# Performance work log

Hardware: AMD Instinct MI355X
Metric: run time of the kernel (lower is better)

## Reference

```python
import jax, jax.numpy as jnp
import numpy as np

N = 100_000      # nodes
E = 1_600_000    # edges (avg degree 16)
C_IN = 128
HID = 128        # 2 * out_channels
OUT = 64
EDIM = 1
NEG_SLOPE = 0.2  # PyG GATConv default negative_slope


def _gat(x, src, dst, n, W, a_s, a_d, b, edge_attr=None, We=None, a_e=None):
    """PyG GATConv with heads=1, concat=True, add_self_loops=True (fill_value='mean').
    x: [n, Cin]; src/dst: [E] (messages flow src -> dst); returns [n, Cout].
    """
    xl = x @ W                 # [n, Cout] transformed node features
    a_src = xl @ a_s           # [n] per-node source attention logit
    a_dst = xl @ a_d           # [n] per-node destination attention logit
    loop = jnp.arange(n)
    if edge_attr is not None:
        # self-loop edge_attr = mean of incoming edge_attr per node (fill_value='mean')
        ones = jnp.ones((src.shape[0],), xl.dtype)
        cnt = jax.ops.segment_sum(ones, dst, num_segments=n)              # [n]
        s = jax.ops.segment_sum(edge_attr, dst, num_segments=n)           # [n, EDIM]
        loop_attr = jnp.where(cnt[:, None] > 0, s / jnp.maximum(cnt, 1.0)[:, None], 0.0)
        ea = jnp.concatenate([edge_attr, loop_attr], axis=0)              # [E+n, EDIM]
    src2 = jnp.concatenate([src, loop])
    dst2 = jnp.concatenate([dst, loop])
    alpha = a_src[src2] + a_dst[dst2]                                      # [E+n]
    if edge_attr is not None:
        alpha = alpha + (ea @ We) @ a_e                                    # edge-attribute attention term
    alpha = jax.nn.leaky_relu(alpha, NEG_SLOPE)
    # softmax over incoming edges of each destination node (stable)
    m = jax.ops.segment_max(alpha, dst2, num_segments=n)
    ex = jnp.exp(alpha - m[dst2])
    den = jax.ops.segment_sum(ex, dst2, num_segments=n)
    coef = ex / den[dst2]                                                  # [E+n]
    out = jax.ops.segment_sum(coef[:, None] * xl[src2], dst2, num_segments=n)
    return out + b


def setup_inputs() -> dict:
    key = jax.random.key(0)
    ks = jax.random.split(key, 32)
    s = 0.1
    inp = {
        "x": jax.random.normal(ks[0], (N, C_IN), jnp.float32),
        "edge_index": jax.random.randint(ks[1], (2, E), 0, N, jnp.int64),
        "edge_weights": jax.random.uniform(ks[2], (E, EDIM), jnp.float32),
    }
    def lin(k, i, o):
        return jax.random.normal(k, (i, o), jnp.float32) * s
    def vec(k, c):
        return jax.random.normal(k, (c,), jnp.float32) * s
    # layer 0: 128 -> 128 (with edge attention)
    inp["W0"], inp["as0"], inp["ad0"] = lin(ks[3], C_IN, HID), vec(ks[4], HID), vec(ks[5], HID)
    inp["ae0"], inp["We0"], inp["b0"] = vec(ks[6], HID), lin(ks[7], EDIM, HID), jnp.zeros((HID,), jnp.float32)
    # layer 1: 128 -> 128 (with edge attention)
    inp["W1"], inp["as1"], inp["ad1"] = lin(ks[8], HID, HID), vec(ks[9], HID), vec(ks[10], HID)
    inp["ae1"], inp["We1"], inp["b1"] = vec(ks[11], HID), lin(ks[12], EDIM, HID), jnp.zeros((HID,), jnp.float32)
    # conv_mu: 128 -> 64 (with edge attention)
    inp["Wm"], inp["asm"], inp["adm"] = lin(ks[13], HID, OUT), vec(ks[14], OUT), vec(ks[15], OUT)
    inp["aem"], inp["Wem"], inp["bm"] = vec(ks[16], OUT), lin(ks[17], EDIM, OUT), jnp.zeros((OUT,), jnp.float32)
    # conv_logstd: 128 -> 64 (called WITHOUT edge_attr -> no edge term)
    inp["Wl"], inp["asl"], inp["adl"] = lin(ks[18], HID, OUT), vec(ks[19], OUT), vec(ks[20], OUT)
    inp["bl"] = jnp.zeros((OUT,), jnp.float32)
    return inp


def reference(x, edge_index, edge_weights,
              W0, as0, ad0, ae0, We0, b0,
              W1, as1, ad1, ae1, We1, b1,
              Wm, asm, adm, aem, Wem, bm,
              Wl, asl, adl, bl):
    src, dst = edge_index[0], edge_index[1]
    h = jax.nn.relu(_gat(x, src, dst, N, W0, as0, ad0, b0, edge_weights, We0, ae0))
    h = jax.nn.relu(_gat(h, src, dst, N, W1, as1, ad1, b1, edge_weights, We1, ae1))
    mu = _gat(h, src, dst, N, Wm, asm, adm, bm, edge_weights, Wem, aem)
    logstd = _gat(h, src, dst, N, Wl, asl, adl, bl)  # no edge_attr, per original forward
    return mu, logstd
```

## Files before the change

### kernel.cpp

```cpp
#include <hip/hip_runtime.h>

#define NN 100000
#define EE 1600000
#define NBK 782
#define NBKP 784
#define NBLK 391
#define NBLKP 392

typedef __attribute__((ext_vector_type(8))) __bf16 bf16x8;
typedef __attribute__((ext_vector_type(4))) float f32x4;
typedef unsigned short u16;

__device__ __forceinline__ float bf2f(u16 v) {
  union { unsigned u; float f; } x; x.u = ((unsigned)v) << 16; return x.f;
}
__device__ __forceinline__ u16 f2bf(float f) {
  union { unsigned u; float f; } x; x.f = f;
  x.u += 0x7fffu + ((x.u >> 16) & 1u);
  return (u16)(x.u >> 16);
}
__device__ __forceinline__ float lo_f(unsigned u) {
  union { unsigned u; float f; } x; x.u = u << 16; return x.f;
}
__device__ __forceinline__ float hi_f(unsigned u) {
  union { unsigned u; float f; } x; x.u = u & 0xffff0000u; return x.f;
}
__device__ __forceinline__ unsigned pack2(float a, float b) {
  return (unsigned)f2bf(a) | ((unsigned)f2bf(b) << 16);
}
__device__ __forceinline__ float lrelu(float x) { return x > 0.f ? x : 0.2f * x; }
__device__ __forceinline__ int clampi(int v, int hi) {
  return ((unsigned)v < (unsigned)hi) ? v : 0;
}
__device__ __forceinline__ float ldf(const void* p, size_t i, int fl) {
  return fl ? ((const float*)p)[i] : bf2f(((const u16*)p)[i]);
}

__device__ __forceinline__ int wave_fdetect(const u16* __restrict__ xb) {
  int lane = threadIdx.x & 63;
  int bad = 0;
#pragma unroll
  for (int j = 0; j < 4; ++j) {
    float a = fabsf(bf2f(xb[lane * 4 + j]));
    bad |= (!(a == a) || a > 1e6f) ? 1 : 0;
  }
  return (__ballot(bad) != 0ull) ? 1 : 0;
}
__device__ __forceinline__ int wave_mdetect(const int* __restrict__ ei) {
  int lane = threadIdx.x & 63;
  int v = (lane < 32) ? ei[2 * lane + 1] : 0;
  return (__ballot(v != 0) == 0ull) ? 1 : 0;
}

__global__ void k_fillf(float* __restrict__ o, int n, float v) {
  int i = blockIdx.x * 256 + threadIdx.x;
  if (i < n) o[i] = v;
}

struct CvtDesc { const void* src; u16* dst; int n; };
struct SetupArgs {
  CvtDesc cvt[12];
  const void* W[4]; u16* WT[4]; int WM[4];
  const void* dw[3]; const void* da[3]; int dm[3];
  float* cvals;
  const u16* xb;
};
__global__ __launch_bounds__(256) void k_setup(SetupArgs a) {
  int b = blockIdx.x, t = threadIdx.x;
  if (b < 12) {
    int fl = wave_fdetect(a.xb);
    const void* src = a.cvt[b].src; u16* dst = a.cvt[b].dst; int n = a.cvt[b].n;
    for (int i = t; i < n; i += 256)
      dst[i] = fl ? f2bf(((const float*)src)[i]) : ((const u16*)src)[i];
    return;
  }
  b -= 12;
  if (b < 192) {
    int fl = wave_fdetect(a.xb);
    int wsel, lb;
    if (b < 64)       { wsel = 0; lb = b; }
    else if (b < 128) { wsel = 1; lb = b - 64; }
    else if (b < 160) { wsel = 2; lb = b - 128; }
    else              { wsel = 3; lb = b - 160; }
    int M = a.WM[wsel];
    int i = lb * 256 + t;
    if (i < 128 * M) {
      int k = i / M, m = i % M;
      a.WT[wsel][m * 128 + k] = f2bf(ldf(a.W[wsel], i, fl));
    }
    return;
  }
  b -= 192;
  if (b < 3) {
    if (t < 64) {
      int fl = wave_fdetect(a.xb);
      float s = 0.f; int m = a.dm[b];
      for (int j = t; j < m; j += 64) s += ldf(a.dw[b], j, fl) * ldf(a.da[b], j, fl);
      for (int off = 32; off; off >>= 1) s += __shfl_xor(s, off);
      if (t == 0) a.cvals[b] = s;
    }
    return;
  }
}

__global__ __launch_bounds__(256) void k_ehist(const int* __restrict__ ei,
                                               int* __restrict__ histM) {
  __shared__ int h[NBKP];
  int blk = blockIdx.x, t = threadIdx.x;
  int m_ = wave_mdetect(ei);
  for (int j = t; j < NBKP; j += 256) h[j] = 0;
  __syncthreads();
#pragma unroll
  for (int j = 0; j < 16; ++j) {
    int e = blk * 4096 + j * 256 + t;
    if (e < EE) {
      int d = m_ ? ei[2 * (size_t)(EE + e)] : ei[EE + e];
      d = clampi(d, NN);
      atomicAdd(&h[d >> 7], 1);
    }
  }
  __syncthreads();
  for (int j = t; j < NBKP; j += 256) histM[j * NBLKP + blk] = h[j];
}

__global__ __launch_bounds__(512) void k_scanA(int* __restrict__ histM,
                                               int* __restrict__ binTot) {
  int b = blockIdx.x, t = threadIdx.x;
  int v = (t < NBLK) ? histM[b * NBLKP + t] : 0;
  int lane = t & 63, w = t >> 6;
  int sc = v;
  for (int off = 1; off < 64; off <<= 1) {
    int o = __shfl_up(sc, off); if (lane >= off) sc += o;
  }
  __shared__ int wt[8];
  if (lane == 63) wt[w] = sc;
  __syncthreads();
  int add = 0;
  for (int k = 0; k < w; ++k) add += wt[k];
  int excl = sc - v + add;
  if (t < NBLK) histM[b * NBLKP + t] = excl;
  if (t == 511) binTot[b] = excl;
}

__global__ __launch_bounds__(256) void k_scanB(const int* __restrict__ binTot,
                                               int* __restrict__ bucketBase,
                                               int* __restrict__ row_off) {
  int t = threadIdx.x;
  int v[4]; int s = 0;
#pragma unroll
  for (int j = 0; j < 4; ++j) {
    int idx = t * 4 + j;
    v[j] = (idx < NBK) ? binTot[idx] : 0;
    s += v[j];
  }
  int lane = t & 63, w = t >> 6;
  int sc = s;
  for (int off = 1; off < 64; off <<= 1) {
    int o = __shfl_up(sc, off); if (lane >= off) sc += o;
  }
  __shared__ int wt[4];
  if (lane == 63) wt[w] = sc;
  __syncthreads();
  int add = 0;
  for (int k = 0; k < w; ++k) add += wt[k];
  int ex = add + sc - s;
#pragma unroll
  for (int j = 0; j < 4; ++j) {
    int idx = t * 4 + j;
    if (idx <= NBK) bucketBase[idx] = ex;
    ex += v[j];
  }
  if (t == 0) row_off[NN] = EE;
}

__global__ __launch_bounds__(256) void k_escatter(
    const int* __restrict__ ei, const void* __restrict__ ew,
    const u16* __restrict__ xb, const int* __restrict__ histM,
    const int* __restrict__ bucketBase, int2* __restrict__ stage) {
  __shared__ int lbase[NBKP];
  __shared__ int cur[NBKP];
  int blk = blockIdx.x, t = threadIdx.x;
  int m_ = wave_mdetect(ei);
  int fl = wave_fdetect(xb);
  for (int j = t; j < NBKP; j += 256) {
    int bb = (j < NBK) ? (bucketBase[j] + histM[j * NBLKP + blk]) : 0;
    lbase[j] = bb; cur[j] = 0;
  }
  __syncthreads();
#pragma unroll
  for (int j = 0; j < 16; ++j) {
    int e = blk * 4096 + j * 256 + t;
    if (e < EE) {
      int s = m_ ? ei[2 * (size_t)e] : ei[e];
      int d = m_ ? ei[2 * (size_t)(EE + e)] : ei[EE + e];
      s = clampi(s, NN);
      d = clampi(d, NN);
      int bin = d >> 7, low = d & 127;
      int r = atomicAdd(&cur[bin], 1);
      int pos = lbase[bin] + r;
      if (pos >= 0 && pos < EE)
        stage[pos] = make_int2(s, (low << 16) | (int)f2bf(ldf(ew, e, fl)));
    }
  }
}

__global__ __launch_bounds__(256) void k_bucket(
    const int2* __restrict__ stage, const int* __restrict__ bucketBase,
    int2* __restrict__ edges, int* __restrict__ row_off, float* __restrict__ la) {
  __shared__ int hist[128];
  __shared__ float wsum[128];
  __shared__ int pref[128];
  __shared__ int cur[128];
  int b = blockIdx.x, t = threadIdx.x;
  int base = bucketBase[b], n = bucketBase[b + 1] - base;
  if (t < 128) { hist[t] = 0; wsum[t] = 0.f; cur[t] = 0; }
  __syncthreads();
  for (int i = t; i < n; i += 256) {
    int2 it = stage[base + i];
    int bin = (it.y >> 16) & 127;
    atomicAdd(&hist[bin], 1);
    atomicAdd(&wsum[bin], bf2f((u16)(it.y & 0xffff)));
  }
  __syncthreads();
  if (t == 0) {
    int run = 0;
    for (int j = 0; j < 128; ++j) { pref[j] = run; run += hist[j]; }
  }
  __syncthreads();
  if (t < 128) {
    int d = b * 128 + t;
    if (d < NN) {
      row_off[d] = base + pref[t];
      la[d] = hist[t] ? wsum[t] / (float)hist[t] : 0.f;
    }
  }
  for (int i = t; i < n; i += 256) {
    int2 it = stage[base + i];
    int bin = (it.y >> 16) & 127;
    int r = atomicAdd(&cur[bin], 1);
    edges[base + pref[bin] + r] = it;
  }
}

template<bool DUAL>
__device__ __forceinline__ void gemm_body(
    int bid, int fl, const void* __restrict__ Araw,
    const u16* __restrict__ WT,
    const u16* __restrict__ avs, const u16* __restrict__ avd,
    u16* __restrict__ xl,
    float* __restrict__ asrc, float* __restrict__ adst,
    float2* __restrict__ asAB, float* __restrict__ adstB, int n) {
  const int K = 128;
  int lane = threadIdx.x & 63;
  int wave = threadIdx.x >> 6;
  int quad = lane >> 4;
  int l16 = lane & 15;
  int r0 = (bid * 4 + wave) * 16;
  if (r0 >= n) return;
  int arow = r0 + l16; if (arow >= n) arow = n - 1;
  bf16x8 afr[4];
  if (fl) {
    const float* af = (const float*)Araw + (size_t)arow * K + quad * 8;
#pragma unroll
    for (int kb = 0; kb < 4; ++kb) {
      float4 f0 = *(const float4*)(af + kb * 32);
      float4 f1 = *(const float4*)(af + kb * 32 + 4);
      union { bf16x8 v; u16 s[8]; } t;
      t.s[0] = f2bf(f0.x); t.s[1] = f2bf(f0.y); t.s[2] = f2bf(f0.z); t.s[3] = f2bf(f0.w);
      t.s[4] = f2bf(f1.x); t.s[5] = f2bf(f1.y); t.s[6] = f2bf(f1.z); t.s[7] = f2bf(f1.w);
      afr[kb] = t.v;
    }
  } else {
    const u16* ab = (const u16*)Araw + (size_t)arow * K + quad * 8;
#pragma unroll
    for (int kb = 0; kb < 4; ++kb) afr[kb] = *(const bf16x8*)(ab + kb * 32);
  }
  f32x4 acc[8];
#pragma unroll
  for (int nb = 0; nb < 8; ++nb) acc[nb] = (f32x4){0.f, 0.f, 0.f, 0.f};
#pragma unroll
  for (int nb = 0; nb < 8; ++nb) {
    const u16* bbase = WT + (size_t)(nb * 16 + l16) * K + quad * 8;
#pragma unroll
    for (int kb = 0; kb < 4; ++kb) {
      bf16x8 bfr = *(const bf16x8*)(bbase + kb * 32);
      acc[nb] = __builtin_amdgcn_mfma_f32_16x16x32_bf16(afr[kb], bfr, acc[nb], 0, 0, 0);
    }
  }
  float ps[2][4] = {{0,0,0,0},{0,0,0,0}}, pd[2][4] = {{0,0,0,0},{0,0,0,0}};
#pragma unroll
  for (int nb = 0; nb < 8; ++nb) {
    const int g = (DUAL && nb >= 4) ? 1 : 0;
    int col = nb * 16 + l16;
    float vs = bf2f(avs[col]), vd = bf2f(avd[col]);
#pragma unroll
    for (int r = 0; r < 4; ++r) {
      int row = r0 + quad * 4 + r;
      float v = acc[nb][r];
      if (row < n) xl[(size_t)row * 128 + col] = f2bf(v);
      ps[g][r] += v * vs;
      pd[g][r] += v * vd;
    }
  }
#pragma unroll
  for (int off = 1; off < 16; off <<= 1) {
#pragma unroll
    for (int r = 0; r < 4; ++r) {
      ps[0][r] += __shfl_xor(ps[0][r], off);
      pd[0][r] += __shfl_xor(pd[0][r], off);
      if (DUAL) {
        ps[1][r] += __shfl_xor(ps[1][r], off);
        pd[1][r] += __shfl_xor(pd[1][r], off);
      }
    }
  }
  if (l16 == 0) {
#pragma unroll
    for (int r = 0; r < 4; ++r) {
      int row = r0 + quad * 4 + r;
      if (row < n) {
        if (DUAL) {
          asAB[row] = make_float2(ps[0][r], ps[1][r]);
          adst[row] = pd[0][r]; adstB[row] = pd[1][r];
        } else {
          asrc[row] = ps[0][r]; adst[row] = pd[0][r];
        }
      }
    }
  }
}

__global__ __launch_bounds__(256) void k_gemm0(
    const u16* __restrict__ xb, const void* __restrict__ Araw,
    const u16* __restrict__ WT, const u16* __restrict__ avs, const u16* __restrict__ avd,
    u16* __restrict__ xl, float* __restrict__ asrc, float* __restrict__ adst, int n) {
  int fl = wave_fdetect(xb);
  gemm_body<false>(blockIdx.x, fl, Araw, WT, avs, avd, xl, asrc, adst,
                   nullptr, nullptr, n);
}

template<bool DUAL>
__global__ __launch_bounds__(256) void k_gemm(
    const u16* __restrict__ A, const u16* __restrict__ WT,
    const u16* __restrict__ avs, const u16* __restrict__ avd,
    u16* __restrict__ xl, float* __restrict__ asrc, float* __restrict__ adst,
    float2* __restrict__ asAB, float* __restrict__ adstB, int n) {
  gemm_body<DUAL>(blockIdx.x, 0, A, WT, avs, avd, xl, asrc, adst, asAB, adstB, n);
}

__global__ __launch_bounds__(256) void k_agg(
    const int* __restrict__ row_off, const int2* __restrict__ edges,
    const float* __restrict__ asrc, const float* __restrict__ adst,
    const float* __restrict__ la, const float* __restrict__ cptr,
    const u16* __restrict__ xl, const u16* __restrict__ bias,
    u16* __restrict__ out, int n) {
  __shared__ float lp[16][16];
  __shared__ int lsv[16][16];
  int tid = blockIdx.x * 256 + threadIdx.x;
  int d = tid >> 4;
  if (d >= n) return;
  int l = threadIdx.x & 15;
  int grp = threadIdx.x >> 4;
  float c = cptr[0];
  float ad = adst[d];
  float aL = lrelu(asrc[d] + ad + c * la[d]);
  float lsum = 0.f;
  int4 su = *(const int4*)(xl + (size_t)d * 128 + l * 8);
  float A0 = lo_f(su.x), A1 = hi_f(su.x), A2 = lo_f(su.y), A3 = hi_f(su.y);
  float A4 = lo_f(su.z), A5 = hi_f(su.z), A6 = lo_f(su.w), A7 = hi_f(su.w);
  float B0 = 0.f, B1 = 0.f, B2 = 0.f, B3 = 0.f, B4 = 0.f, B5 = 0.f, B6 = 0.f, B7 = 0.f;
  int beg = row_off[d], end = row_off[d + 1];
  for (int base = beg; base < end; base += 16) {
    int i = base + l;
    bool v = i < end;
    int2 ev = v ? edges[i] : make_int2(0, 0);
    float e = 0.f;
    if (v) e = __expf(lrelu(asrc[ev.x] + ad + c * bf2f((u16)(ev.y & 0xffff))) - aL);
    lsum += e;
    lp[grp][l] = e; lsv[grp][l] = ev.x;
    int cnt = end - base; if (cnt > 16) cnt = 16;
    int j = 0;
    for (; j + 2 <= cnt; j += 2) {
      float p0 = lp[grp][j];     int s0 = lsv[grp][j];
      float p1 = lp[grp][j + 1]; int s1 = lsv[grp][j + 1];
      int4 u0 = *(const int4*)(xl + (size_t)s0 * 128 + l * 8);
      int4 u1 = *(const int4*)(xl + (size_t)s1 * 128 + l * 8);
      A0 = fmaf(p0, lo_f(u0.x), A0); A1 = fmaf(p0, hi_f(u0.x), A1);
      A2 = fmaf(p0, lo_f(u0.y), A2); A3 = fmaf(p0, hi_f(u0.y), A3);
      A4 = fmaf(p0, lo_f(u0.z), A4); A5 = fmaf(p0, hi_f(u0.z), A5);
      A6 = fmaf(p0, lo_f(u0.w), A6); A7 = fmaf(p0, hi_f(u0.w), A7);
      B0 = fmaf(p1, lo_f(u1.x), B0); B1 = fmaf(p1, hi_f(u1.x), B1);
      B2 = fmaf(p1, lo_f(u1.y), B2); B3 = fmaf(p1, hi_f(u1.y), B3);
      B4 = fmaf(p1, lo_f(u1.z), B4); B5 = fmaf(p1, hi_f(u1.z), B5);
      B6 = fmaf(p1, lo_f(u1.w), B6); B7 = fmaf(p1, hi_f(u1.w), B7);
    }
    if (j < cnt) {
      float p0 = lp[grp][j]; int s0 = lsv[grp][j];
      int4 u0 = *(const int4*)(xl + (size_t)s0 * 128 + l * 8);
      A0 = fmaf(p0, lo_f(u0.x), A0); A1 = fmaf(p0, hi_f(u0.x), A1);
      A2 = fmaf(p0, lo_f(u0.y), A2); A3 = fmaf(p0, hi_f(u0.y), A3);
      A4 = fmaf(p0, lo_f(u0.z), A4); A5 = fmaf(p0, hi_f(u0.z), A5);
      A6 = fmaf(p0, lo_f(u0.w), A6); A7 = fmaf(p0, hi_f(u0.w), A7);
    }
  }
  A0 += B0; A1 += B1; A2 += B2; A3 += B3; A4 += B4; A5 += B5; A6 += B6; A7 += B7;
#pragma unroll
  for (int off = 1; off < 16; off <<= 1) lsum += __shfl_xor(lsum, off);
  float inv = 1.f / (lsum + 1.f);
  int4 bv = *(const int4*)(bias + l * 8);
  float o0 = fmaxf(fmaf(A0, inv, lo_f((unsigned)bv.x)), 0.f);
  float o1 = fmaxf(fmaf(A1, inv, hi_f((unsigned)bv.x)), 0.f);
  float o2 = fmaxf(fmaf(A2, inv, lo_f((unsigned)bv.y)), 0.f);
  float o3 = fmaxf(fmaf(A3, inv, hi_f((unsigned)bv.y)), 0.f);
  float o4 = fmaxf(fmaf(A4, inv, lo_f((unsigned)bv.z)), 0.f);
  float o5 = fmaxf(fmaf(A5, inv, hi_f((unsigned)bv.z)), 0.f);
  float o6 = fmaxf(fmaf(A6, inv, lo_f((unsigned)bv.w)), 0.f);
  float o7 = fmaxf(fmaf(A7, inv, hi_f((unsigned)bv.w)), 0.f);
  int4 ov;
  ov.x = (int)pack2(o0, o1); ov.y = (int)pack2(o2, o3);
  ov.z = (int)pack2(o4, o5); ov.w = (int)pack2(o6, o7);
  *(int4*)(out + (size_t)d * 128 + l * 8) = ov;
}

__global__ __launch_bounds__(256) void k_aggh(
    const int* __restrict__ row_off, const int2* __restrict__ edges,
    const float2* __restrict__ asAB, const float* __restrict__ adA,
    const float* __restrict__ adB,
    const float* __restrict__ la, const float* __restrict__ cptr,
    const u16* __restrict__ xl, const u16* __restrict__ bias,
    float* __restrict__ outf, int n) {
  __shared__ float lpA[16][16];
  __shared__ float lpB[16][16];
  __shared__ int lsv[16][16];
  int tid = blockIdx.x * 256 + threadIdx.x;
  int d = tid >> 4;
  if (d >= n) return;
  int l = threadIdx.x & 15;
  int grp = threadIdx.x >> 4;
  bool isMu = l < 8;
  float c = cptr[0];
  float adAd = adA[d], adBd = adB[d];
  float2 abd = asAB[d];
  float aLA = lrelu(abd.x + adAd + c * la[d]);
  float aLB = lrelu(abd.y + adBd);
  float lsA = 0.f, lsB = 0.f;
  int4 su = *(const int4*)(xl + (size_t)d * 128 + l * 8);
  float A0 = lo_f(su.x), A1 = hi_f(su.x), A2 = lo_f(su.y), A3 = hi_f(su.y);
  float A4 = lo_f(su.z), A5 = hi_f(su.z), A6 = lo_f(su.w), A7 = hi_f(su.w);
  float B0 = 0.f, B1 = 0.f, B2 = 0.f, B3 = 0.f, B4 = 0.f, B5 = 0.f, B6 = 0.f, B7 = 0.f;
  int beg = row_off[d], end = row_off[d + 1];
  for (int base = beg; base < end; base += 16) {
    int i = base + l;
    bool v = i < end;
    int2 ev = v ? edges[i] : make_int2(0, 0);
    float eA = 0.f, eB = 0.f;
    if (v) {
      float2 ab = asAB[ev.x];
      eA = __expf(lrelu(ab.x + adAd + c * bf2f((u16)(ev.y & 0xffff))) - aLA);
      eB = __expf(lrelu(ab.y + adBd) - aLB);
    }
    lsA += eA; lsB += eB;
    lpA[grp][l] = eA; lpB[grp][l] = eB; lsv[grp][l] = ev.x;
    const float* lpp = isMu ? lpA[grp] : lpB[grp];
    int cnt = end - base; if (cnt > 16) cnt = 16;
    int j = 0;
    for (; j + 2 <= cnt; j += 2) {
      float p0 = lpp[j];     int s0 = lsv[grp][j];
      float p1 = lpp[j + 1]; int s1 = lsv[grp][j + 1];
      int4 u0 = *(const int4*)(xl + (size_t)s0 * 128 + l * 8);
      int4 u1 = *(const int4*)(xl + (size_t)s1 * 128 + l * 8);
      A0 = fmaf(p0, lo_f(u0.x), A0); A1 = fmaf(p0, hi_f(u0.x), A1);
      A2 = fmaf(p0, lo_f(u0.y), A2); A3 = fmaf(p0, hi_f(u0.y), A3);
      A4 = fmaf(p0, lo_f(u0.z), A4); A5 = fmaf(p0, hi_f(u0.z), A5);
      A6 = fmaf(p0, lo_f(u0.w), A6); A7 = fmaf(p0, hi_f(u0.w), A7);
      B0 = fmaf(p1, lo_f(u1.x), B0); B1 = fmaf(p1, hi_f(u1.x), B1);
      B2 = fmaf(p1, lo_f(u1.y), B2); B3 = fmaf(p1, hi_f(u1.y), B3);
      B4 = fmaf(p1, lo_f(u1.z), B4); B5 = fmaf(p1, hi_f(u1.z), B5);
      B6 = fmaf(p1, lo_f(u1.w), B6); B7 = fmaf(p1, hi_f(u1.w), B7);
    }
    if (j < cnt) {
      float p0 = lpp[j]; int s0 = lsv[grp][j];
      int4 u0 = *(const int4*)(xl + (size_t)s0 * 128 + l * 8);
      A0 = fmaf(p0, lo_f(u0.x), A0); A1 = fmaf(p0, hi_f(u0.x), A1);
      A2 = fmaf(p0, lo_f(u0.y), A2); A3 = fmaf(p0, hi_f(u0.y), A3);
      A4 = fmaf(p0, lo_f(u0.z), A4); A5 = fmaf(p0, hi_f(u0.z), A5);
      A6 = fmaf(p0, lo_f(u0.w), A6); A7 = fmaf(p0, hi_f(u0.w), A7);
    }
  }
  A0 += B0; A1 += B1; A2 += B2; A3 += B3; A4 += B4; A5 += B5; A6 += B6; A7 += B7;
#pragma unroll
  for (int off = 1; off < 16; off <<= 1) {
    lsA += __shfl_xor(lsA, off);
    lsB += __shfl_xor(lsB, off);
  }
  float inv = 1.f / ((isMu ? lsA : lsB) + 1.f);
  int4 bv = *(const int4*)(bias + l * 8);
  float4 oa, ob;
  oa.x = fmaf(A0, inv, lo_f((unsigned)bv.x));
  oa.y = fmaf(A1, inv, hi_f((unsigned)bv.x));
  oa.z = fmaf(A2, inv, lo_f((unsigned)bv.y));
  oa.w = fmaf(A3, inv, hi_f((unsigned)bv.y));
  ob.x = fmaf(A4, inv, lo_f((unsigned)bv.z));
  ob.y = fmaf(A5, inv, hi_f((unsigned)bv.z));
  ob.z = fmaf(A6, inv, lo_f((unsigned)bv.w));
  ob.w = fmaf(A7, inv, hi_f((unsigned)bv.w));
  float* obase = isMu ? (outf + (size_t)d * 64 + l * 8)
                      : (outf + (size_t)NN * 64 + (size_t)d * 64 + (l - 8) * 8);
  *(float4*)obase = oa;
  *(float4*)(obase + 4) = ob;
}

extern "C" void kernel_launch(void* const* d_in, const int* in_sizes, int n_in,
                              void* d_out, int out_size, void* d_ws, size_t ws_size,
                              hipStream_t stream) {
  (void)in_sizes; (void)n_in;
  const int* ei = (const int*)d_in[1];
  const u16* xb = (const u16*)d_in[0];
  float* outf = (float*)d_out;

  u16* regionA = (u16*)d_out;
  u16* regionB = (u16*)d_out + (size_t)NN * 128;
  int* histM = (int*)d_out;

  char* p = (char*)d_ws;
  auto alloc = [&](size_t bytes) -> char* {
    char* r = p; p += (bytes + 255) & ~(size_t)255; return r;
  };
  int*   row_off   = (int*)alloc((NN + 1) * 4);
  int*   binTot    = (int*)alloc(NBKP * 4);
  int*   bucketBase= (int*)alloc((NBKP + 2) * 4);
  float* la        = (float*)alloc(NN * 4);
  float* asrcA     = (float*)alloc(NN * 4);
  float* adstA     = (float*)alloc(NN * 4);
  float* adstB     = (float*)alloc(NN * 4);
  float2* asAB     = (float2*)alloc((size_t)NN * 8);
  int2*  edges     = (int2*)alloc((size_t)EE * 8);
  u16*   WT0       = (u16*)alloc(128 * 128 * 2);
  u16*   WT1       = (u16*)alloc(128 * 128 * 2);
  u16*   WTh       = (u16*)alloc(128 * 128 * 2);
  float* cvals     = (float*)alloc(16);
  u16*   vecc      = (u16*)alloc(9 * 256);
  u16*   xl        = (u16*)alloc((size_t)NN * 128 * 2);

  int2* stage = (int2*)xl;

  size_t NEED = (size_t)(p - (char*)d_ws);
  if (ws_size < NEED) {
    k_fillf<<<(out_size + 255) / 256, 256, 0, stream>>>(outf, out_size, 0.125f);
    return;
  }

  u16* as0c = vecc + 0 * 128; u16* ad0c = vecc + 1 * 128; u16* b0c = vecc + 2 * 128;
  u16* as1c = vecc + 3 * 128; u16* ad1c = vecc + 4 * 128; u16* b1c = vecc + 5 * 128;
  u16* hvs  = vecc + 6 * 128; u16* hvd  = vecc + 7 * 128; u16* bh  = vecc + 8 * 128;

  SetupArgs sa;
  sa.cvt[0]  = {d_in[4],  as0c, 128};
  sa.cvt[1]  = {d_in[5],  ad0c, 128};
  sa.cvt[2]  = {d_in[8],  b0c,  128};
  sa.cvt[3]  = {d_in[10], as1c, 128};
  sa.cvt[4]  = {d_in[11], ad1c, 128};
  sa.cvt[5]  = {d_in[14], b1c,  128};
  sa.cvt[6]  = {d_in[16], hvs,      64};
  sa.cvt[7]  = {d_in[22], hvs + 64, 64};
  sa.cvt[8]  = {d_in[17], hvd,      64};
  sa.cvt[9]  = {d_in[23], hvd + 64, 64};
  sa.cvt[10] = {d_in[20], bh,       64};
  sa.cvt[11] = {d_in[24], bh + 64,  64};
  sa.W[0] = d_in[3];  sa.WT[0] = WT0;            sa.WM[0] = 128;
  sa.W[1] = d_in[9];  sa.WT[1] = WT1;            sa.WM[1] = 128;
  sa.W[2] = d_in[15]; sa.WT[2] = WTh;            sa.WM[2] = 64;
  sa.W[3] = d_in[21]; sa.WT[3] = WTh + 64 * 128; sa.WM[3] = 64;
  sa.dw[0] = d_in[7];  sa.da[0] = d_in[6];  sa.dm[0] = 128;
  sa.dw[1] = d_in[13]; sa.da[1] = d_in[12]; sa.dm[1] = 128;
  sa.dw[2] = d_in[19]; sa.da[2] = d_in[18]; sa.dm[2] = 64;
  sa.cvals = cvals; sa.xb = xb;
  k_setup<<<12 + 192 + 3, 256, 0, stream>>>(sa);

  const int gblocks = (((NN + 15) / 16) + 3) / 4;
  const int eblocks16 = (int)(((size_t)NN * 16 + 255) / 256);

  k_ehist<<<NBLK, 256, 0, stream>>>(ei, histM);
  k_scanA<<<NBK, 512, 0, stream>>>(histM, binTot);
  k_scanB<<<1, 256, 0, stream>>>(binTot, bucketBase, row_off);
  k_escatter<<<NBLK, 256, 0, stream>>>(ei, d_in[2], xb, histM, bucketBase, stage);
  k_bucket<<<NBK, 256, 0, stream>>>(stage, bucketBase, edges, row_off, la);

  k_gemm0<<<gblocks, 256, 0, stream>>>(xb, d_in[0], WT0, as0c, ad0c,
                                       xl, asrcA, adstA, NN);
  k_agg<<<eblocks16, 256, 0, stream>>>(row_off, edges, asrcA, adstA, la,
                                       cvals + 0, xl, b0c, regionB, NN);
  k_gemm<false><<<gblocks, 256, 0, stream>>>(regionB, WT1, as1c, ad1c,
                                             xl, asrcA, adstA, nullptr, nullptr, NN);
  k_agg<<<eblocks16, 256, 0, stream>>>(row_off, edges, asrcA, adstA, la,
                                       cvals + 1, xl, b1c, regionA, NN);
  k_gemm<true><<<gblocks, 256, 0, stream>>>(regionA, WTh, hvs, hvd,
                                            xl, nullptr, adstA, asAB, adstB, NN);
  k_aggh<<<eblocks16, 256, 0, stream>>>(row_off, edges, asAB, adstA, adstB,
                                        la, cvals + 2, xl, bh, outf, NN);
}
```

Baseline: 526.2 us.

## Merge edge histogram into setup and edge scatter with first GEMM launch

Folds the edge-destination histogram blocks into the setup kernel and runs the edge scatter alongside the first-layer GEMM in one launch, which cuts two kernel launches and lets independent work share the GPU. The stage buffer moves from the xl workspace into the output region so the scatter and the GEMM writing xl do not collide. The aggregation kernels also gain a 4-way unrolled gather loop for more memory-level parallelism. Risks include the stage buffer overlapping histM or other output data, and higher register pressure from the wider unroll.

```diff
diff --git a/kernel.cpp b/kernel.cpp
--- a/kernel.cpp
+++ b/kernel.cpp
@@ -6,6 +6,7 @@
 #define NBKP 784
 #define NBLK 391
 #define NBLKP 392
+#define SETB 207
 
 typedef __attribute__((ext_vector_type(8))) __bf16 bf16x8;
 typedef __attribute__((ext_vector_type(4))) float f32x4;
@@ -64,9 +65,30 @@
   const void* dw[3]; const void* da[3]; int dm[3];
   float* cvals;
   const u16* xb;
+  const int* ei;
+  int* histM;
 };
 __global__ __launch_bounds__(256) void k_setup(SetupArgs a) {
+  __shared__ int h[NBKP];
   int b = blockIdx.x, t = threadIdx.x;
+  if (b >= SETB) {
+    int blk = b - SETB;
+    int m_ = wave_mdetect(a.ei);
+    for (int j = t; j < NBKP; j += 256) h[j] = 0;
+    __syncthreads();
+#pragma unroll
+    for (int j = 0; j < 16; ++j) {
+      int e = blk * 4096 + j * 256 + t;
+      if (e < EE) {
+        int d = m_ ? a.ei[2 * (size_t)(EE + e)] : a.ei[EE + e];
+        d = clampi(d, NN);
+        atomicAdd(&h[d >> 7], 1);
+      }
+    }
+    __syncthreads();
+    for (int j = t; j < NBKP; j += 256) a.histM[j * NBLKP + blk] = h[j];
+    return;
+  }
   if (b < 12) {
     int fl = wave_fdetect(a.xb);
     const void* src = a.cvt[b].src; u16* dst = a.cvt[b].dst; int n = a.cvt[b].n;
@@ -103,26 +125,6 @@
   }
 }
 
-__global__ __launch_bounds__(256) void k_ehist(const int* __restrict__ ei,
-                                               int* __restrict__ histM) {
-  __shared__ int h[NBKP];
-  int blk = blockIdx.x, t = threadIdx.x;
-  int m_ = wave_mdetect(ei);
-  for (int j = t; j < NBKP; j += 256) h[j] = 0;
-  __syncthreads();
-#pragma unroll
-  for (int j = 0; j < 16; ++j) {
-    int e = blk * 4096 + j * 256 + t;
-    if (e < EE) {
-      int d = m_ ? ei[2 * (size_t)(EE + e)] : ei[EE + e];
-      d = clampi(d, NN);
-      atomicAdd(&h[d >> 7], 1);
-    }
-  }
-  __syncthreads();
-  for (int j = t; j < NBKP; j += 256) histM[j * NBLKP + blk] = h[j];
-}
-
 __global__ __launch_bounds__(512) void k_scanA(int* __restrict__ histM,
                                                int* __restrict__ binTot) {
   int b = blockIdx.x, t = threadIdx.x;
@@ -171,75 +173,6 @@
     ex += v[j];
   }
   if (t == 0) row_off[NN] = EE;
-}
-
-__global__ __launch_bounds__(256) void k_escatter(
-    const int* __restrict__ ei, const void* __restrict__ ew,
-    const u16* __restrict__ xb, const int* __restrict__ histM,
-    const int* __restrict__ bucketBase, int2* __restrict__ stage) {
-  __shared__ int lbase[NBKP];
-  __shared__ int cur[NBKP];
-  int blk = blockIdx.x, t = threadIdx.x;
-  int m_ = wave_mdetect(ei);
-  int fl = wave_fdetect(xb);
-  for (int j = t; j < NBKP; j += 256) {
-    int bb = (j < NBK) ? (bucketBase[j] + histM[j * NBLKP + blk]) : 0;
-    lbase[j] = bb; cur[j] = 0;
-  }
-  __syncthreads();
-#pragma unroll
-  for (int j = 0; j < 16; ++j) {
-    int e = blk * 4096 + j * 256 + t;
-    if (e < EE) {
-      int s = m_ ? ei[2 * (size_t)e] : ei[e];
-      int d = m_ ? ei[2 * (size_t)(EE + e)] : ei[EE + e];
-      s = clampi(s, NN);
-      d = clampi(d, NN);
-      int bin = d >> 7, low = d & 127;
-      int r = atomicAdd(&cur[bin], 1);
-      int pos = lbase[bin] + r;
-      if (pos >= 0 && pos < EE)
-        stage[pos] = make_int2(s, (low << 16) | (int)f2bf(ldf(ew, e, fl)));
-    }
-  }
-}
-
-__global__ __launch_bounds__(256) void k_bucket(
-    const int2* __restrict__ stage, const int* __restrict__ bucketBase,
-    int2* __restrict__ edges, int* __restrict__ row_off, float* __restrict__ la) {
-  __shared__ int hist[128];
-  __shared__ float wsum[128];
-  __shared__ int pref[128];
-  __shared__ int cur[128];
-  int b = blockIdx.x, t = threadIdx.x;
-  int base = bucketBase[b], n = bucketBase[b + 1] - base;
-  if (t < 128) { hist[t] = 0; wsum[t] = 0.f; cur[t] = 0; }
-  __syncthreads();
-  for (int i = t; i < n; i += 256) {
-    int2 it = stage[base + i];
-    int bin = (it.y >> 16) & 127;
-    atomicAdd(&hist[bin], 1);
-    atomicAdd(&wsum[bin], bf2f((u16)(it.y & 0xffff)));
-  }
-  __syncthreads();
-  if (t == 0) {
-    int run = 0;
-    for (int j = 0; j < 128; ++j) { pref[j] = run; run += hist[j]; }
-  }
-  __syncthreads();
-  if (t < 128) {
-    int d = b * 128 + t;
-    if (d < NN) {
-      row_off[d] = base + pref[t];
-      la[d] = hist[t] ? wsum[t] / (float)hist[t] : 0.f;
-    }
-  }
-  for (int i = t; i < n; i += 256) {
-    int2 it = stage[base + i];
-    int bin = (it.y >> 16) & 127;
-    int r = atomicAdd(&cur[bin], 1);
-    edges[base + pref[bin] + r] = it;
-  }
 }
 
 template<bool DUAL>
@@ -330,13 +263,82 @@
   }
 }
 
-__global__ __launch_bounds__(256) void k_gemm0(
-    const u16* __restrict__ xb, const void* __restrict__ Araw,
-    const u16* __restrict__ WT, const u16* __restrict__ avs, const u16* __restrict__ avd,
+__global__ __launch_bounds__(256) void k_esgemm(
+    const int* __restrict__ ei, const void* __restrict__ ew,
+    const u16* __restrict__ xb, const int* __restrict__ histM,
+    const int* __restrict__ bucketBase, int2* __restrict__ stage,
+    const void* __restrict__ Araw, const u16* __restrict__ WT,
+    const u16* __restrict__ avs, const u16* __restrict__ avd,
     u16* __restrict__ xl, float* __restrict__ asrc, float* __restrict__ adst, int n) {
+  __shared__ int lbase[NBKP];
+  __shared__ int cur[NBKP];
+  if ((int)blockIdx.x >= NBLK) {
+    int fl = wave_fdetect(xb);
+    gemm_body<false>((int)blockIdx.x - NBLK, fl, Araw, WT, avs, avd,
+                     xl, asrc, adst, nullptr, nullptr, n);
+    return;
+  }
+  int blk = blockIdx.x, t = threadIdx.x;
+  int m_ = wave_mdetect(ei);
   int fl = wave_fdetect(xb);
-  gemm_body<false>(blockIdx.x, fl, Araw, WT, avs, avd, xl, asrc, adst,
-                   nullptr, nullptr, n);
+  for (int j = t; j < NBKP; j += 256) {
+    int bb = (j < NBK) ? (bucketBase[j] + histM[j * NBLKP + blk]) : 0;
+    lbase[j] = bb; cur[j] = 0;
+  }
+  __syncthreads();
+#pragma unroll
+  for (int j = 0; j < 16; ++j) {
+    int e = blk * 4096 + j * 256 + t;
+    if (e < EE) {
+      int s = m_ ? ei[2 * (size_t)e] : ei[e];
+      int d = m_ ? ei[2 * (size_t)(EE + e)] : ei[EE + e];
+      s = clampi(s, NN);
+      d = clampi(d, NN);
+      int bin = d >> 7, low = d & 127;
+      int r = atomicAdd(&cur[bin], 1);
+      int pos = lbase[bin] + r;
+      if (pos >= 0 && pos < EE)
+        stage[pos] = make_int2(s, (low << 16) | (int)f2bf(ldf(ew, e, fl)));
+    }
+  }
+}
+
+__global__ __launch_bounds__(256) void k_bucket(
+    const int2* __restrict__ stage, const int* __restrict__ bucketBase,
+    int2* __restrict__ edges, int* __restrict__ row_off, float* __restrict__ la) {
+  __shared__ int hist[128];
+  __shared__ float wsum[128];
+  __shared__ int pref[128];
+  __shared__ int cur[128];
+  int b = blockIdx.x, t = threadIdx.x;
+  int base = bucketBase[b], n = bucketBase[b + 1] - base;
+  if (t < 128) { hist[t] = 0; wsum[t] = 0.f; cur[t] = 0; }
+  __syncthreads();
+  for (int i = t; i < n; i += 256) {
+    int2 it = stage[base + i];
+    int bin = (it.y >> 16) & 127;
+    atomicAdd(&hist[bin], 1);
+    atomicAdd(&wsum[bin], bf2f((u16)(it.y & 0xffff)));
+  }
+  __syncthreads();
+  if (t == 0) {
+    int run = 0;
+    for (int j = 0; j < 128; ++j) { pref[j] = run; run += hist[j]; }
+  }
+  __syncthreads();
+  if (t < 128) {
+    int d = b * 128 + t;
+    if (d < NN) {
+      row_off[d] = base + pref[t];
+      la[d] = hist[t] ? wsum[t] / (float)hist[t] : 0.f;
+    }
+  }
+  for (int i = t; i < n; i += 256) {
+    int2 it = stage[base + i];
+    int bin = (it.y >> 16) & 127;
+    int r = atomicAdd(&cur[bin], 1);
+    edges[base + pref[bin] + r] = it;
+  }
 }
 
 template<bool DUAL>
@@ -380,6 +382,32 @@
     lp[grp][l] = e; lsv[grp][l] = ev.x;
     int cnt = end - base; if (cnt > 16) cnt = 16;
     int j = 0;
+    for (; j + 4 <= cnt; j += 4) {
+      float p0 = lp[grp][j + 0]; int s0 = lsv[grp][j + 0];
+      float p1 = lp[grp][j + 1]; int s1 = lsv[grp][j + 1];
+      float p2 = lp[grp][j + 2]; int s2 = lsv[grp][j + 2];
+      float p3 = lp[grp][j + 3]; int s3 = lsv[grp][j + 3];
+      int4 u0 = *(const int4*)(xl + (size_t)s0 * 128 + l * 8);
+      int4 u1 = *(const int4*)(xl + (size_t)s1 * 128 + l * 8);
+      int4 u2 = *(const int4*)(xl + (size_t)s2 * 128 + l * 8);
+      int4 u3 = *(const int4*)(xl + (size_t)s3 * 128 + l * 8);
+      A0 = fmaf(p0, lo_f(u0.x), A0); A1 = fmaf(p0, hi_f(u0.x), A1);
+      A2 = fmaf(p0, lo_f(u0.y), A2); A3 = fmaf(p0, hi_f(u0.y), A3);
+      A4 = fmaf(p0, lo_f(u0.z), A4); A5 = fmaf(p0, hi_f(u0.z), A5);
+      A6 = fmaf(p0, lo_f(u0.w), A6); A7 = fmaf(p0, hi_f(u0.w), A7);
+      B0 = fmaf(p1, lo_f(u1.x), B0); B1 = fmaf(p1, hi_f(u1.x), B1);
+      B2 = fmaf(p1, lo_f(u1.y), B2); B3 = fmaf(p1, hi_f(u1.y), B3);
+      B4 = fmaf(p1, lo_f(u1.z), B4); B5 = fmaf(p1, hi_f(u1.z), B5);
+      B6 = fmaf(p1, lo_f(u1.w), B6); B7 = fmaf(p1, hi_f(u1.w), B7);
+      A0 = fmaf(p2, lo_f(u2.x), A0); A1 = fmaf(p2, hi_f(u2.x), A1);
+      A2 = fmaf(p2, lo_f(u2.y), A2); A3 = fmaf(p2, hi_f(u2.y), A3);
+      A4 = fmaf(p2, lo_f(u2.z), A4); A5 = fmaf(p2, hi_f(u2.z), A5);
+      A6 = fmaf(p2, lo_f(u2.w), A6); A7 = fmaf(p2, hi_f(u2.w), A7);
+      B0 = fmaf(p3, lo_f(u3.x), B0); B1 = fmaf(p3, hi_f(u3.x), B1);
+      B2 = fmaf(p3, lo_f(u3.y), B2); B3 = fmaf(p3, hi_f(u3.y), B3);
+      B4 = fmaf(p3, lo_f(u3.z), B4); B5 = fmaf(p3, hi_f(u3.z), B5);
+      B6 = fmaf(p3, lo_f(u3.w), B6); B7 = fmaf(p3, hi_f(u3.w), B7);
+    }
     for (; j + 2 <= cnt; j += 2) {
       float p0 = lp[grp][j];     int s0 = lsv[grp][j];
       float p1 = lp[grp][j + 1]; int s1 = lsv[grp][j + 1];
@@ -464,6 +492,32 @@
     const float* lpp = isMu ? lpA[grp] : lpB[grp];
     int cnt = end - base; if (cnt > 16) cnt = 16;
     int j = 0;
+    for (; j + 4 <= cnt; j += 4) {
+      float p0 = lpp[j + 0]; int s0 = lsv[grp][j + 0];
+      float p1 = lpp[j + 1]; int s1 = lsv[grp][j + 1];
+      float p2 = lpp[j + 2]; int s2 = lsv[grp][j + 2];
+      float p3 = lpp[j + 3]; int s3 = lsv[grp][j + 3];
+      int4 u0 = *(const int4*)(xl + (size_t)s0 * 128 + l * 8);
+      int4 u1 = *(const int4*)(xl + (size_t)s1 * 128 + l * 8);
+      int4 u2 = *(const int4*)(xl + (size_t)s2 * 128 + l * 8);
+      int4 u3 = *(const int4*)(xl + (size_t)s3 * 128 + l * 8);
+      A0 = fmaf(p0, lo_f(u0.x), A0); A1 = fmaf(p0, hi_f(u0.x), A1);
+      A2 = fmaf(p0, lo_f(u0.y), A2); A3 = fmaf(p0, hi_f(u0.y), A3);
+      A4 = fmaf(p0, lo_f(u0.z), A4); A5 = fmaf(p0, hi_f(u0.z), A5);
+      A6 = fmaf(p0, lo_f(u0.w), A6); A7 = fmaf(p0, hi_f(u0.w), A7);
+      B0 = fmaf(p1, lo_f(u1.x), B0); B1 = fmaf(p1, hi_f(u1.x), B1);
+      B2 = fmaf(p1, lo_f(u1.y), B2); B3 = fmaf(p1, hi_f(u1.y), B3);
+      B4 = fmaf(p1, lo_f(u1.z), B4); B5 = fmaf(p1, hi_f(u1.z), B5);
+      B6 = fmaf(p1, lo_f(u1.w), B6); B7 = fmaf(p1, hi_f(u1.w), B7);
+      A0 = fmaf(p2, lo_f(u2.x), A0); A1 = fmaf(p2, hi_f(u2.x), A1);
+      A2 = fmaf(p2, lo_f(u2.y), A2); A3 = fmaf(p2, hi_f(u2.y), A3);
+      A4 = fmaf(p2, lo_f(u2.z), A4); A5 = fmaf(p2, hi_f(u2.z), A5);
+      A6 = fmaf(p2, lo_f(u2.w), A6); A7 = fmaf(p2, hi_f(u2.w), A7);
+      B0 = fmaf(p3, lo_f(u3.x), B0); B1 = fmaf(p3, hi_f(u3.x), B1);
+      B2 = fmaf(p3, lo_f(u3.y), B2); B3 = fmaf(p3, hi_f(u3.y), B3);
+      B4 = fmaf(p3, lo_f(u3.z), B4); B5 = fmaf(p3, hi_f(u3.z), B5);
+      B6 = fmaf(p3, lo_f(u3.w), B6); B7 = fmaf(p3, hi_f(u3.w), B7);
+    }
     for (; j + 2 <= cnt; j += 2) {
       float p0 = lpp[j];     int s0 = lsv[grp][j];
       float p1 = lpp[j + 1]; int s1 = lsv[grp][j + 1];
@@ -521,6 +575,7 @@
   u16* regionA = (u16*)d_out;
   u16* regionB = (u16*)d_out + (size_t)NN * 128;
   int* histM = (int*)d_out;
+  int2* stage = (int2*)((char*)d_out + (size_t)2 * 1024 * 1024);
 
   char* p = (char*)d_ws;
   auto alloc = [&](size_t bytes) -> char* {
@@ -541,8 +596,6 @@
   float* cvals     = (float*)alloc(16);
   u16*   vecc      = (u16*)alloc(9 * 256);
   u16*   xl        = (u16*)alloc((size_t)NN * 128 * 2);
-
-  int2* stage = (int2*)xl;
 
   size_t NEED = (size_t)(p - (char*)d_ws);
   if (ws_size < NEED) {
@@ -574,20 +627,19 @@
   sa.dw[0] = d_in[7];  sa.da[0] = d_in[6];  sa.dm[0] = 128;
   sa.dw[1] = d_in[13]; sa.da[1] = d_in[12]; sa.dm[1] = 128;
   sa.dw[2] = d_in[19]; sa.da[2] = d_in[18]; sa.dm[2] = 64;
-  sa.cvals = cvals; sa.xb = xb;
-  k_setup<<<12 + 192 + 3, 256, 0, stream>>>(sa);
+  sa.cvals = cvals; sa.xb = xb; sa.ei = ei; sa.histM = histM;
+  k_setup<<<SETB + NBLK, 256, 0, stream>>>(sa);
 
   const int gblocks = (((NN + 15) / 16) + 3) / 4;
   const int eblocks16 = (int)(((size_t)NN * 16 + 255) / 256);
 
-  k_ehist<<<NBLK, 256, 0, stream>>>(ei, histM);
   k_scanA<<<NBK, 512, 0, stream>>>(histM, binTot);
   k_scanB<<<1, 256, 0, stream>>>(binTot, bucketBase, row_off);
-  k_escatter<<<NBLK, 256, 0, stream>>>(ei, d_in[2], xb, histM, bucketBase, stage);
+  k_esgemm<<<NBLK + gblocks, 256, 0, stream>>>(ei, d_in[2], xb, histM, bucketBase,
+                                               stage, d_in[0], WT0, as0c, ad0c,
+                                               xl, asrcA, adstA, NN);
   k_bucket<<<NBK, 256, 0, stream>>>(stage, bucketBase, edges, row_off, la);
 
-  k_gemm0<<<gblocks, 256, 0, stream>>>(xb, d_in[0], WT0, as0c, ad0c,
-                                       xl, asrcA, adstA, NN);
   k_agg<<<eblocks16, 256, 0, stream>>>(row_off, edges, asrcA, adstA, la,
                                        cvals + 0, xl, b0c, regionB, NN);
   k_gemm<false><<<gblocks, 256, 0, stream>>>(regionB, WT1, as1c, ad1c,
```

New measurement: 515.2 us (median of 2 runs). 1.02x faster.
